# Performance work log

Measured on AMD Instinct MI355X. Metric: run time of the kernel, lower is better.

The kernel has to match this reference:

```python
import jax, jax.numpy as jnp
import numpy as np

N_NODES = 50000


def setup_inputs() -> dict:
    key = jax.random.key(0)
    k1, k2, k3, k4, k5, k6 = jax.random.split(key, 6)
    N, E, DIN, DOUT = N_NODES, 800000, 256, 256
    h = jax.random.normal(k1, (N, DIN), dtype=jnp.float32)
    e_w = jax.random.uniform(k2, (E, 1), dtype=jnp.float32)
    src = jax.random.randint(k3, (E,), 0, N, dtype=jnp.int32)
    dst = jax.random.randint(k4, (E,), 0, N, dtype=jnp.int32)
    stdv = 1.0 / np.sqrt(DOUT)
    weight = jax.random.uniform(k5, (DIN, DOUT), dtype=jnp.float32, minval=-stdv, maxval=stdv)
    bias = jax.random.uniform(k6, (DOUT,), dtype=jnp.float32, minval=-stdv, maxval=stdv)
    return {"h": h, "e_w": e_w, "src": src, "dst": dst, "weight": weight, "bias": bias}


def reference(h, e_w, src, dst, weight, bias):
    # u_mul_e: message m_e = h[src_e] * x_e  (edge weight broadcast over feature dim)
    m = h[src] * e_w                      # [E, DIN]
    # sum('m','h'): scatter-add messages to destination nodes
    agg = jax.ops.segment_sum(m, dst, num_segments=h.shape[0])  # [N, DIN]
    # dense GEMM + bias
    return agg @ weight + bias            # [N, DOUT]
```

## Files before the change

kernel.cpp:

```cpp
#include <hip/hip_runtime.h>
#include <hip/hip_bf16.h>


#define DIN 256
#define DOUT 256
#define CAP 64

typedef short bf16x8 __attribute__((ext_vector_type(8)));
typedef float f32x4  __attribute__((ext_vector_type(4)));
typedef unsigned short ushort8v __attribute__((ext_vector_type(8)));
typedef unsigned short ushort4v __attribute__((ext_vector_type(4)));
typedef int int4v __attribute__((ext_vector_type(4)));
typedef float f4v __attribute__((ext_vector_type(4)));

__device__ __forceinline__ unsigned short f2bf(float f) {
    unsigned u = __float_as_uint(f);
    u = (u + 0x7FFF + ((u >> 16) & 1)) >> 16;
    return (unsigned short)u;
}
__device__ __forceinline__ float bf2f(unsigned short s) {
    return __uint_as_float(((unsigned)s) << 16);
}

__global__ __launch_bounds__(256) void prep_kernel(const float* __restrict__ W,
                                                   unsigned short* __restrict__ WTfrag,
                                                   int* __restrict__ cursors, int N) {
    int gid = blockIdx.x * 256 + threadIdx.x;
    if (gid < 16 * 8 * 64) {
        int lane = gid & 63;
        int tc = gid >> 6;
        int c = tc & 7;
        int t = tc >> 3;
        int q = lane >> 4, l16 = lane & 15;
        int col = t * 16 + l16;
        int krow = c * 32 + q * 8;
        ushort8v v;
#pragma unroll
        for (int j = 0; j < 8; ++j) v[j] = f2bf(W[(size_t)(krow + j) * DOUT + col]);
        *(ushort8v*)(WTfrag + (size_t)gid * 8) = v;
    }
    for (int i = gid; i < N; i += gridDim.x * 256) cursors[i] = 0;
}

__global__ __launch_bounds__(256) void fill_kernel(const int* __restrict__ src,
                                                   const int* __restrict__ dst,
                                                   const float* __restrict__ e_w,
                                                   int* __restrict__ cursors,
                                                   int2* __restrict__ slots, int E) {
    int e = (blockIdx.x * 256 + threadIdx.x) * 4;
    if (e + 3 < E) {
        int4v s = __builtin_nontemporal_load((const int4v*)(src + e));
        int4v d = __builtin_nontemporal_load((const int4v*)(dst + e));
        f4v  w = __builtin_nontemporal_load((const f4v*)(e_w + e));
        int p0 = atomicAdd(&cursors[d[0]], 1);
        int p1 = atomicAdd(&cursors[d[1]], 1);
        int p2 = atomicAdd(&cursors[d[2]], 1);
        int p3 = atomicAdd(&cursors[d[3]], 1);
        if (p0 < CAP) slots[(size_t)d[0] * CAP + p0] = make_int2(s[0], __float_as_int(w[0]));
        if (p1 < CAP) slots[(size_t)d[1] * CAP + p1] = make_int2(s[1], __float_as_int(w[1]));
        if (p2 < CAP) slots[(size_t)d[2] * CAP + p2] = make_int2(s[2], __float_as_int(w[2]));
        if (p3 < CAP) slots[(size_t)d[3] * CAP + p3] = make_int2(s[3], __float_as_int(w[3]));
    } else {
        for (; e < E; ++e) {
            int d0 = dst[e];
            int pos = atomicAdd(&cursors[d0], 1);
            if (pos < CAP) slots[(size_t)d0 * CAP + pos] = make_int2(src[e], __float_as_int(e_w[e]));
        }
    }
}

__global__ __launch_bounds__(256, 2) void gemm_mfma_kernel(const float* __restrict__ h,
                                                           const unsigned short* __restrict__ WTfrag,
                                                           unsigned short* __restrict__ hW,
                                                           int M, int ntiles) {
    __shared__ unsigned short Af[4 * 8 * 64 * 8];

    int tid  = threadIdx.x;
    int wave = tid >> 6;
    int lane = tid & 63;
    int quad = lane >> 4;
    int l16  = lane & 15;

    bf16x8 breg[4][8];
#pragma unroll
    for (int tq = 0; tq < 4; ++tq)
#pragma unroll
        for (int c = 0; c < 8; ++c)
            breg[tq][c] = *(const bf16x8*)(WTfrag +
                ((size_t)((wave * 4 + tq) * 8 + c) * 64 + lane) * 8);

    for (int tile = blockIdx.x; tile < ntiles; tile += gridDim.x) {
        int row0 = tile * 64;
        __syncthreads();
#pragma unroll
        for (int j = 0; j < 16; ++j) {
            int flat = j * 256 + tid;
            int row  = flat >> 6;
            int col4 = (flat & 63) << 2;
            int r = row0 + row;
            float4 f = make_float4(0.f, 0.f, 0.f, 0.f);
            if (r < M) f = *(const float4*)(h + (size_t)r * DIN + col4);
            int w = row >> 4, l16r = row & 15;
            int c = col4 >> 5, q = (col4 >> 3) & 3, jj = col4 & 7;
            ushort4v u;
            u[0] = f2bf(f.x); u[1] = f2bf(f.y); u[2] = f2bf(f.z); u[3] = f2bf(f.w);
            *(ushort4v*)&Af[(size_t)(((w * 8 + c) * 64 + q * 16 + l16r) << 3) + jj] = u;
        }
        __syncthreads();

#pragma unroll
        for (int s = 0; s < 4; ++s) {
            f32x4 acc[4];
#pragma unroll
            for (int tq = 0; tq < 4; ++tq) acc[tq] = (f32x4){0.f, 0.f, 0.f, 0.f};
#pragma unroll
            for (int c = 0; c < 8; ++c) {
                bf16x8 a = *(const bf16x8*)&Af[(size_t)((s * 8 + c) * 64 + lane) * 8];
#pragma unroll
                for (int tq = 0; tq < 4; ++tq)
                    acc[tq] = __builtin_amdgcn_mfma_f32_16x16x32_bf16(a, breg[tq][c], acc[tq], 0, 0, 0);
            }
            int r0 = row0 + s * 16;
#pragma unroll
            for (int tq = 0; tq < 4; ++tq) {
#pragma unroll
                for (int r = 0; r < 4; ++r) {
                    int row = r0 + quad * 4 + r;
                    if (row < M)
                        hW[(size_t)row * DOUT + (wave * 4 + tq) * 16 + l16] = f2bf(acc[tq][r]);
                }
            }
        }
    }
}

__global__ __launch_bounds__(256) void gather_kernel(const unsigned short* __restrict__ hW,
                                                     const int2* __restrict__ slots,
                                                     const int* __restrict__ cursors,
                                                     const float* __restrict__ bias,
                                                     float* __restrict__ out,
                                                     int node0, int cnt, int N) {
    int node = node0 + blockIdx.x * 4 + (threadIdx.x >> 6);
    if (node >= node0 + cnt || node >= N) return;
    int lane = threadIdx.x & 63;
    int len  = cursors[node];
    if (len > CAP) len = CAP;
    const int4v* sl4 = (const int4v*)(slots + (size_t)node * CAP);
    const unsigned short* hp = hW + lane * 4;

    float a0 = 0.f, a1 = 0.f, a2 = 0.f, a3 = 0.f;
    int i = 0;
    for (; i + 8 <= len; i += 8) {
        int4v q0 = __builtin_nontemporal_load(sl4 + (i >> 1) + 0);
        int4v q1 = __builtin_nontemporal_load(sl4 + (i >> 1) + 1);
        int4v q2 = __builtin_nontemporal_load(sl4 + (i >> 1) + 2);
        int4v q3 = __builtin_nontemporal_load(sl4 + (i >> 1) + 3);
        ushort4v v0 = *(const ushort4v*)(hp + ((size_t)(unsigned)q0[0] << 8));
        ushort4v v1 = *(const ushort4v*)(hp + ((size_t)(unsigned)q0[2] << 8));
        ushort4v v2 = *(const ushort4v*)(hp + ((size_t)(unsigned)q1[0] << 8));
        ushort4v v3 = *(const ushort4v*)(hp + ((size_t)(unsigned)q1[2] << 8));
        ushort4v v4 = *(const ushort4v*)(hp + ((size_t)(unsigned)q2[0] << 8));
        ushort4v v5 = *(const ushort4v*)(hp + ((size_t)(unsigned)q2[2] << 8));
        ushort4v v6 = *(const ushort4v*)(hp + ((size_t)(unsigned)q3[0] << 8));
        ushort4v v7 = *(const ushort4v*)(hp + ((size_t)(unsigned)q3[2] << 8));
        float w0 = __int_as_float(q0[1]), w1 = __int_as_float(q0[3]);
        float w2 = __int_as_float(q1[1]), w3 = __int_as_float(q1[3]);
        float w4 = __int_as_float(q2[1]), w5 = __int_as_float(q2[3]);
        float w6 = __int_as_float(q3[1]), w7 = __int_as_float(q3[3]);
        a0 += w0 * bf2f(v0[0]) + w1 * bf2f(v1[0]) + w2 * bf2f(v2[0]) + w3 * bf2f(v3[0])
            + w4 * bf2f(v4[0]) + w5 * bf2f(v5[0]) + w6 * bf2f(v6[0]) + w7 * bf2f(v7[0]);
        a1 += w0 * bf2f(v0[1]) + w1 * bf2f(v1[1]) + w2 * bf2f(v2[1]) + w3 * bf2f(v3[1])
            + w4 * bf2f(v4[1]) + w5 * bf2f(v5[1]) + w6 * bf2f(v6[1]) + w7 * bf2f(v7[1]);
        a2 += w0 * bf2f(v0[2]) + w1 * bf2f(v1[2]) + w2 * bf2f(v2[2]) + w3 * bf2f(v3[2])
            + w4 * bf2f(v4[2]) + w5 * bf2f(v5[2]) + w6 * bf2f(v6[2]) + w7 * bf2f(v7[2]);
        a3 += w0 * bf2f(v0[3]) + w1 * bf2f(v1[3]) + w2 * bf2f(v2[3]) + w3 * bf2f(v3[3])
            + w4 * bf2f(v4[3]) + w5 * bf2f(v5[3]) + w6 * bf2f(v6[3]) + w7 * bf2f(v7[3]);
    }
    for (; i + 2 <= len; i += 2) {
        int4v q = __builtin_nontemporal_load(sl4 + (i >> 1));
        ushort4v u0 = *(const ushort4v*)(hp + ((size_t)(unsigned)q[0] << 8));
        ushort4v u1 = *(const ushort4v*)(hp + ((size_t)(unsigned)q[2] << 8));
        float w0 = __int_as_float(q[1]), w1 = __int_as_float(q[3]);
        a0 += w0 * bf2f(u0[0]) + w1 * bf2f(u1[0]);
        a1 += w0 * bf2f(u0[1]) + w1 * bf2f(u1[1]);
        a2 += w0 * bf2f(u0[2]) + w1 * bf2f(u1[2]);
        a3 += w0 * bf2f(u0[3]) + w1 * bf2f(u1[3]);
    }
    if (i < len) {
        int2 m = slots[(size_t)node * CAP + i];
        float w = __int_as_float(m.y);
        ushort4v u = *(const ushort4v*)(hp + ((size_t)(unsigned)m.x << 8));
        a0 += w * bf2f(u[0]);
        a1 += w * bf2f(u[1]);
        a2 += w * bf2f(u[2]);
        a3 += w * bf2f(u[3]);
    }

    float4 b = *(const float4*)(bias + lane * 4);
    f32x4 v;
    v[0] = a0 + b.x; v[1] = a1 + b.y; v[2] = a2 + b.z; v[3] = a3 + b.w;
    __builtin_nontemporal_store(v, (f32x4*)(out + (size_t)node * DOUT + lane * 4));
}

extern "C" void kernel_launch(void* const* d_in, const int* in_sizes, int n_in,
                              void* d_out, int out_size, void* d_ws, size_t ws_size,
                              hipStream_t stream) {
    const float* h    = (const float*)d_in[0];
    const float* e_w  = (const float*)d_in[1];
    const int*   src  = (const int*)d_in[2];
    const int*   dst  = (const int*)d_in[3];
    const float* W    = (const float*)d_in[4];
    const float* bias = (const float*)d_in[5];
    float* out = (float*)d_out;

    int N = in_sizes[0] / DIN;
    int E = in_sizes[1];
    int ntiles = (N + 63) / 64;

    char* base = (char*)d_ws;
    unsigned short* WTfrag = (unsigned short*)base;
    size_t off = (size_t)DIN * DOUT * sizeof(unsigned short);
    unsigned short* hW = (unsigned short*)(base + off);
    off += (size_t)N * DOUT * sizeof(unsigned short);
    int* cursors = (int*)(base + off);
    off += (size_t)N * sizeof(int);
    off = (off + 15) & ~(size_t)15;
    int2* slots = (int2*)(base + off);
    off += (size_t)N * CAP * sizeof(int2);

    prep_kernel<<<64, 256, 0, stream>>>(W, WTfrag, cursors, N);
    fill_kernel<<<(E / 4 + 255) / 256, 256, 0, stream>>>(src, dst, e_w, cursors, slots, E);
    gemm_mfma_kernel<<<512, 256, 0, stream>>>(h, WTfrag, hW, N, ntiles);
    int half = (N + 1) / 2;
    gather_kernel<<<(half + 3) / 4, 256, 0, stream>>>(hW, slots, cursors, bias, out, 0, half, N);
    gather_kernel<<<(N - half + 3) / 4, 256, 0, stream>>>(hW, slots, cursors, bias, out, half, N - half, N);
}
```

Measured before the change: 241.6 us.

## Fuse edge-bucketing fill and bf16 GEMM into one role-split launch

Combines the edge-bucketing fill kernel and the MFMA GEMM into a single launch of 1536 blocks. Every third block runs a GEMM tile loop with a fixed stride of 512, and the other two blocks in each group bucket edges. The atomic-heavy scatter and the compute/streaming GEMM can therefore run on the GPU at the same time instead of one after the other. The two half-size gather launches are also merged into one launch over all nodes. The trade-off is that fill blocks now carry the GEMM's shared-memory allocation and register budget, which may lower their occupancy. Many of the fill blocks past the last edge are also launched and do no work.

```diff
diff --git a/kernel.cpp b/kernel.cpp
--- a/kernel.cpp
+++ b/kernel.cpp
@@ -42,39 +42,46 @@
     for (int i = gid; i < N; i += gridDim.x * 256) cursors[i] = 0;
 }
 
-__global__ __launch_bounds__(256) void fill_kernel(const int* __restrict__ src,
-                                                   const int* __restrict__ dst,
-                                                   const float* __restrict__ e_w,
-                                                   int* __restrict__ cursors,
-                                                   int2* __restrict__ slots, int E) {
-    int e = (blockIdx.x * 256 + threadIdx.x) * 4;
-    if (e + 3 < E) {
-        int4v s = __builtin_nontemporal_load((const int4v*)(src + e));
-        int4v d = __builtin_nontemporal_load((const int4v*)(dst + e));
-        f4v  w = __builtin_nontemporal_load((const f4v*)(e_w + e));
-        int p0 = atomicAdd(&cursors[d[0]], 1);
-        int p1 = atomicAdd(&cursors[d[1]], 1);
-        int p2 = atomicAdd(&cursors[d[2]], 1);
-        int p3 = atomicAdd(&cursors[d[3]], 1);
-        if (p0 < CAP) slots[(size_t)d[0] * CAP + p0] = make_int2(s[0], __float_as_int(w[0]));
-        if (p1 < CAP) slots[(size_t)d[1] * CAP + p1] = make_int2(s[1], __float_as_int(w[1]));
-        if (p2 < CAP) slots[(size_t)d[2] * CAP + p2] = make_int2(s[2], __float_as_int(w[2]));
-        if (p3 < CAP) slots[(size_t)d[3] * CAP + p3] = make_int2(s[3], __float_as_int(w[3]));
-    } else {
-        for (; e < E; ++e) {
-            int d0 = dst[e];
-            int pos = atomicAdd(&cursors[d0], 1);
-            if (pos < CAP) slots[(size_t)d0 * CAP + pos] = make_int2(src[e], __float_as_int(e_w[e]));
+__global__ __launch_bounds__(256, 2) void fused_kernel(const float* __restrict__ h,
+                                                       const unsigned short* __restrict__ WTfrag,
+                                                       unsigned short* __restrict__ hW,
+                                                       int M, int ntiles,
+                                                       const int* __restrict__ src,
+                                                       const int* __restrict__ dst,
+                                                       const float* __restrict__ e_w,
+                                                       int* __restrict__ cursors,
+                                                       int2* __restrict__ slots, int E) {
+    __shared__ unsigned short Af[4 * 8 * 64 * 8];
+
+    int b = blockIdx.x;
+    int role = b % 3;
+
+    if (role != 0) {
+        int fb = (b / 3) * 2 + role - 1;
+        int e = (fb * 256 + (int)threadIdx.x) * 4;
+        if (e + 3 < E) {
+            int4v s = __builtin_nontemporal_load((const int4v*)(src + e));
+            int4v d = __builtin_nontemporal_load((const int4v*)(dst + e));
+            f4v  w = __builtin_nontemporal_load((const f4v*)(e_w + e));
+            int p0 = atomicAdd(&cursors[d[0]], 1);
+            int p1 = atomicAdd(&cursors[d[1]], 1);
+            int p2 = atomicAdd(&cursors[d[2]], 1);
+            int p3 = atomicAdd(&cursors[d[3]], 1);
+            if (p0 < CAP) slots[(size_t)d[0] * CAP + p0] = make_int2(s[0], __float_as_int(w[0]));
+            if (p1 < CAP) slots[(size_t)d[1] * CAP + p1] = make_int2(s[1], __float_as_int(w[1]));
+            if (p2 < CAP) slots[(size_t)d[2] * CAP + p2] = make_int2(s[2], __float_as_int(w[2]));
+            if (p3 < CAP) slots[(size_t)d[3] * CAP + p3] = make_int2(s[3], __float_as_int(w[3]));
+        } else {
+            for (; e < E; ++e) {
+                int d0 = dst[e];
+                int pos = atomicAdd(&cursors[d0], 1);
+                if (pos < CAP) slots[(size_t)d0 * CAP + pos] = make_int2(src[e], __float_as_int(e_w[e]));
+            }
         }
-    }
-}
-
-__global__ __launch_bounds__(256, 2) void gemm_mfma_kernel(const float* __restrict__ h,
-                                                           const unsigned short* __restrict__ WTfrag,
-                                                           unsigned short* __restrict__ hW,
-                                                           int M, int ntiles) {
-    __shared__ unsigned short Af[4 * 8 * 64 * 8];
-
+        return;
+    }
+
+    int gb = b / 3;
     int tid  = threadIdx.x;
     int wave = tid >> 6;
     int lane = tid & 63;
@@ -89,7 +96,7 @@
             breg[tq][c] = *(const bf16x8*)(WTfrag +
                 ((size_t)((wave * 4 + tq) * 8 + c) * 64 + lane) * 8);
 
-    for (int tile = blockIdx.x; tile < ntiles; tile += gridDim.x) {
+    for (int tile = gb; tile < ntiles; tile += 512) {
         int row0 = tile * 64;
         __syncthreads();
 #pragma unroll
@@ -138,10 +145,9 @@
                                                      const int2* __restrict__ slots,
                                                      const int* __restrict__ cursors,
                                                      const float* __restrict__ bias,
-                                                     float* __restrict__ out,
-                                                     int node0, int cnt, int N) {
-    int node = node0 + blockIdx.x * 4 + (threadIdx.x >> 6);
-    if (node >= node0 + cnt || node >= N) return;
+                                                     float* __restrict__ out, int N) {
+    int node = blockIdx.x * 4 + (threadIdx.x >> 6);
+    if (node >= N) return;
     int lane = threadIdx.x & 63;
     int len  = cursors[node];
     if (len > CAP) len = CAP;
@@ -229,9 +235,7 @@
     off += (size_t)N * CAP * sizeof(int2);
 
     prep_kernel<<<64, 256, 0, stream>>>(W, WTfrag, cursors, N);
-    fill_kernel<<<(E / 4 + 255) / 256, 256, 0, stream>>>(src, dst, e_w, cursors, slots, E);
-    gemm_mfma_kernel<<<512, 256, 0, stream>>>(h, WTfrag, hW, N, ntiles);
-    int half = (N + 1) / 2;
-    gather_kernel<<<(half + 3) / 4, 256, 0, stream>>>(hW, slots, cursors, bias, out, 0, half, N);
-    gather_kernel<<<(N - half + 3) / 4, 256, 0, stream>>>(hW, slots, cursors, bias, out, half, N - half, N);
-}
+    fused_kernel<<<1536, 256, 0, stream>>>(h, WTfrag, hW, N, ntiles,
+                                           src, dst, e_w, cursors, slots, E);
+    gather_kernel<<<(N + 3) / 4, 256, 0, stream>>>(hW, slots, cursors, bias, out, N);
+}
```

Result: faster. 220.4 us (-8.8%).
